# Optimization experiments

Measured on AMD Instinct MI355X. Metric: run time of the kernel, lower is better.

The kernel has to match this reference:

```python
import jax, jax.numpy as jnp
import numpy as np


def setup_inputs() -> dict:
    key = jax.random.key(0)
    k1, k2 = jax.random.split(key)
    B, S, D, E = 4, 8192, 1024, 64
    x = jax.random.normal(k1, (B, S, D), dtype=jnp.float32)
    W = jax.random.normal(k2, (E, D), dtype=jnp.float32) * (1.0 / np.sqrt(D))
    return {"x": x, "W": W, "top_k": 1}


EXPERT_CAPACITY = 640


def reference(x, W, top_k):
    # Router logits: small-dim linear (bias=False), jitter=0 so no noise.
    logits = jnp.einsum("bsd,ed->bse", x, W)              # [B,S,E]
    probs = jax.nn.softmax(logits, axis=-1)               # [B,S,E]
    num_experts = W.shape[0]
    # top-k over experts (top_k == 1 here)
    top_k_values, top_k_indices = jax.lax.top_k(probs, top_k)  # [B,S,k]
    # one-hot over experts, summed over the k slots -> [B,S,E] int mask
    expert_indices = jax.nn.one_hot(top_k_indices, num_experts, dtype=jnp.int32).sum(axis=-2)
    # token priority: running count of tokens assigned to each expert along seq
    token_priority = jnp.cumsum(expert_indices, axis=-2)  # [B,S,E]
    capacity_mask = token_priority <= EXPERT_CAPACITY
    expert_indices = expert_indices * capacity_mask.astype(jnp.int32)
    # top_k_values [B,S,1] broadcasts over E (valid only for k==1, as in torch)
    router_probs = top_k_values * expert_indices.astype(top_k_values.dtype)
    return expert_indices, router_probs, logits
```

## Files before the change

kernel.cpp:

```cpp
#include <hip/hip_runtime.h>
#include <hip/hip_bf16.h>

#define NB 4
#define NS 8192
#define ND 1024
#define NE 64
#define NM (NB * NS)
#define CAPACITY 640

#define BM 64
#define BK 64
#define NKT (ND / BK)
#define NBLK (NM / BM)
#define CPB (NS / BM)

#define OCH 64
#define NOB (NM / OCH)

typedef short short8 __attribute__((ext_vector_type(8)));
typedef float f32x4 __attribute__((ext_vector_type(4)));

#define GLOAD16(g, l)                                                          \
    __builtin_amdgcn_global_load_lds(                                          \
        (const __attribute__((address_space(1))) void*)(g),                    \
        (__attribute__((address_space(3))) void*)(l), 16, 0, 0)

__global__ __launch_bounds__(256, 2) void k1_mfma(const float* __restrict__ x,
                                                  const float* __restrict__ W,
                                                  float* __restrict__ logits,
                                                  int* __restrict__ idx_ws,
                                                  float* __restrict__ prob_ws,
                                                  int* __restrict__ hist)
{
    __shared__ char SL[65536];
    __shared__ int lh[NE];

    const int tid = threadIdx.x;
    const int lane = tid & 63;
    const int wv = tid >> 6;
    const int lr = lane & 15;
    const int kq = lane >> 4;
    const int tok0 = blockIdx.x * BM;

    if (tid < NE) lh[tid] = 0;

    f32x4 acc[4];
#pragma unroll
    for (int j = 0; j < 4; ++j) acc[j] = (f32x4){0.f, 0.f, 0.f, 0.f};

    auto stage = [&](int kt, int b) {
        const int k0 = kt * BK;
        const int half = wv & 1;
        const int r0 = half * 32 + (lane >> 4);
        const int uslot = lane & 15;
        const float* src;
        char* dst;
        if (wv < 2) {
            src = x + (size_t)(tok0)*ND;
            dst = SL + b * 16384 + half * 8192;
        } else {
            src = W;
            dst = SL + 32768 + b * 16384 + half * 8192;
        }
#pragma unroll
        for (int i = 0; i < 8; ++i) {
            const int r = r0 + i * 4;
            const int su = uslot ^ (r & 15);
            const float* g = src + (size_t)r * ND + k0 + su * 4;
            GLOAD16(g, dst + i * 1024);
        }
    };

    auto compute = [&](int b) {
        const float* xsb = (const float*)(SL + b * 16384);
        const float* wsb = (const float*)(SL + 32768 + b * 16384);
        const int arow = wv * 16 + lr;
#pragma unroll
        for (int kk = 0; kk < 2; ++kk) {
            const int su = kk * 8 + kq * 2;
            f32x4 a0 = *(const f32x4*)&xsb[arow * 64 + ((su)     ^ lr) * 4];
            f32x4 a1 = *(const f32x4*)&xsb[arow * 64 + ((su + 1) ^ lr) * 4];
            float f[8] = {a0[0], a0[1], a0[2], a0[3], a1[0], a1[1], a1[2], a1[3]};
            short8 ah, al;
#pragma unroll
            for (int c = 0; c < 8; ++c) {
                unsigned int u = __builtin_bit_cast(unsigned int, f[c]);
                ah[c] = (short)(u >> 16);
                float fhi = __builtin_bit_cast(float, u & 0xFFFF0000u);
                __hip_bfloat16 lb = __float2bfloat16(f[c] - fhi);
                al[c] = __builtin_bit_cast(short, lb);
            }
#pragma unroll
            for (int j = 0; j < 4; ++j) {
                const int erow = j * 16 + lr;
                f32x4 w0 = *(const f32x4*)&wsb[erow * 64 + ((su)     ^ lr) * 4];
                f32x4 w1 = *(const f32x4*)&wsb[erow * 64 + ((su + 1) ^ lr) * 4];
                float g[8] = {w0[0], w0[1], w0[2], w0[3], w1[0], w1[1], w1[2], w1[3]};
                short8 bh, bl;
#pragma unroll
                for (int c = 0; c < 8; ++c) {
                    __hip_bfloat16 hb = __float2bfloat16(g[c]);
                    float r = g[c] - __bfloat162float(hb);
                    __hip_bfloat16 lb = __float2bfloat16(r);
                    bh[c] = __builtin_bit_cast(short, hb);
                    bl[c] = __builtin_bit_cast(short, lb);
                }
                acc[j] = __builtin_amdgcn_mfma_f32_16x16x32_bf16(ah, bh, acc[j], 0, 0, 0);
                acc[j] = __builtin_amdgcn_mfma_f32_16x16x32_bf16(ah, bl, acc[j], 0, 0, 0);
                acc[j] = __builtin_amdgcn_mfma_f32_16x16x32_bf16(al, bh, acc[j], 0, 0, 0);
            }
        }
    };

    stage(0, 0);
#pragma unroll
    for (int kt = 0; kt < NKT; ++kt) {
        const int b = kt & 1;
        if (kt + 1 < NKT) {
            stage(kt + 1, b ^ 1);
            asm volatile("s_waitcnt vmcnt(8)" ::: "memory");
        } else {
            asm volatile("s_waitcnt vmcnt(0)" ::: "memory");
        }
        __builtin_amdgcn_s_barrier();
        __builtin_amdgcn_sched_barrier(0);
        compute(b);
        __builtin_amdgcn_sched_barrier(0);
        __builtin_amdgcn_s_barrier();
    }

    __syncthreads();

    float* sLog = (float*)SL;

#pragma unroll
    for (int r = 0; r < 4; ++r) {
        const int tl = wv * 16 + kq * 4 + r;
        float val[4];
#pragma unroll
        for (int j = 0; j < 4; ++j) val[j] = acc[j][r];

        float m = val[0];
        int mi = lr;
#pragma unroll
        for (int j = 1; j < 4; ++j) {
            if (val[j] > m) { m = val[j]; mi = j * 16 + lr; }
        }
#pragma unroll
        for (int off = 1; off < 16; off <<= 1) {
            float m2 = __shfl_xor(m, off);
            int mi2 = __shfl_xor(mi, off);
            if (m2 > m || (m2 == m && mi2 < mi)) { m = m2; mi = mi2; }
        }
        float s = 0.0f;
#pragma unroll
        for (int j = 0; j < 4; ++j) s += __expf(val[j] - m);
#pragma unroll
        for (int off = 1; off < 16; off <<= 1) s += __shfl_xor(s, off);

#pragma unroll
        for (int j = 0; j < 4; ++j) sLog[tl * NE + j * 16 + lr] = val[j];
        if (lr == 0) {
            idx_ws[tok0 + tl] = mi;
            prob_ws[tok0 + tl] = 1.0f / s;
            atomicAdd(&lh[mi], 1);
        }
    }
    __syncthreads();

    const size_t g0 = (size_t)tok0 * NE;
#pragma unroll
    for (int i = 0; i < 4; ++i) {
        const int fl = i * 1024 + tid * 4;
        *(float4*)&logits[g0 + fl] = *(const float4*)&sLog[fl];
    }
    if (tid < NE) hist[blockIdx.x * NE + tid] = lh[tid];
}

__global__ __launch_bounds__(256) void k_out(const int* __restrict__ idx_ws,
                                             const float* __restrict__ prob_ws,
                                             const int* __restrict__ hist,
                                             float* __restrict__ e_out,
                                             float* __restrict__ p_out)
{
    __shared__ int sMi[OCH];
    __shared__ float sPr[OCH];
    __shared__ int sAd[OCH];
    __shared__ int pp[4][NE];

    const int c = blockIdx.x;
    const int b = c >> 7;
    const int s = c & 127;
    const int t0 = c * OCH;
    const int tid = threadIdx.x;
    const int lane = tid & 63;
    const int wv = tid >> 6;

    if (tid < OCH) {
        sMi[tid] = idx_ws[t0 + tid];
        sPr[tid] = prob_ws[t0 + tid];
    }

    {
        int run = 0;
        const int* hrow = hist + (size_t)(b * CPB) * NE + lane;
        for (int i = wv; i < s; i += 4) run += hrow[i * NE];
        pp[wv][lane] = run;
    }
    __syncthreads();

    if (wv == 0) {
        int run = pp[0][lane] + pp[1][lane] + pp[2][lane] + pp[3][lane];
        for (int j = 0; j < OCH; ++j) {
            if (sMi[j] == lane) { ++run; sAd[j] = (run <= CAPACITY) ? 1 : 0; }
        }
    }
    __syncthreads();

    const size_t g0 = (size_t)t0 * NE;
#pragma unroll
    for (int i = 0; i < 4; ++i) {
        const int fl = i * 1024 + tid * 4;
        const int t = fl >> 6;
        const int e0 = fl & 63;
        const int mi = sMi[t];
        const float pr = sPr[t];
        const int ad = sAd[t];
        float4 ev, pv;
        float* evp = &ev.x;
        float* pvp = &pv.x;
#pragma unroll
        for (int cc = 0; cc < 4; ++cc) {
            const bool hit = (mi == e0 + cc) && ad;
            evp[cc] = hit ? 1.0f : 0.0f;
            pvp[cc] = hit ? pr : 0.0f;
        }
        *(float4*)&e_out[g0 + fl] = ev;
        *(float4*)&p_out[g0 + fl] = pv;
    }
}

extern "C" void kernel_launch(void* const* d_in, const int* in_sizes, int n_in,
                              void* d_out, int out_size, void* d_ws, size_t ws_size,
                              hipStream_t stream)
{
    const float* x = (const float*)d_in[0];
    const float* W = (const float*)d_in[1];

    float* out = (float*)d_out;
    float* e_out = out;
    float* p_out = out + (size_t)NM * NE;
    float* logits = out + 2 * (size_t)NM * NE;

    char* ws = (char*)d_ws;
    int* idx_ws    = (int*)ws;
    float* prob_ws = (float*)(ws + (size_t)NM * 4);
    int* hist      = (int*)(ws + (size_t)NM * 8);

    k1_mfma<<<NBLK, 256, 0, stream>>>(x, W, logits, idx_ws, prob_ws, hist);
    k_out<<<NOB, 256, 0, stream>>>(idx_ws, prob_ws, hist, e_out, p_out);
}
```

Measured before the change: 47.01 us.

## Shrink GEMM tile to 32 tokens with 32-wide K and two-wave blocks

Reduces the router GEMM block from 64 tokens with four waves to 32 tokens with two waves and a 32-wide K step. The staging map, LDS swizzle and logits write-out are reworked to match, and the histogram prefix in the output kernel now sums twice as many per-block entries. The aim is more blocks and higher occupancy with less LDS per block. In exchange W is re-read from global/L2 twice as often per token, and there are twice as many K iterations with barriers.

```diff
diff --git a/kernel.cpp b/kernel.cpp
--- a/kernel.cpp
+++ b/kernel.cpp
@@ -8,11 +8,11 @@
 #define NM (NB * NS)
 #define CAPACITY 640
 
-#define BM 64
-#define BK 64
+#define BM 32
+#define BK 32
 #define NKT (ND / BK)
 #define NBLK (NM / BM)
-#define CPB (NS / BM)
+#define C32PB (NS / BM)
 
 #define OCH 64
 #define NOB (NM / OCH)
@@ -25,14 +25,14 @@
         (const __attribute__((address_space(1))) void*)(g),                    \
         (__attribute__((address_space(3))) void*)(l), 16, 0, 0)
 
-__global__ __launch_bounds__(256, 2) void k1_mfma(const float* __restrict__ x,
+__global__ __launch_bounds__(128, 4) void k1_mfma(const float* __restrict__ x,
                                                   const float* __restrict__ W,
                                                   float* __restrict__ logits,
                                                   int* __restrict__ idx_ws,
                                                   float* __restrict__ prob_ws,
                                                   int* __restrict__ hist)
 {
-    __shared__ char SL[65536];
+    __shared__ char SL[24576];
     __shared__ int lh[NE];
 
     const int tid = threadIdx.x;
@@ -50,65 +50,62 @@
 
     auto stage = [&](int kt, int b) {
         const int k0 = kt * BK;
-        const int half = wv & 1;
-        const int r0 = half * 32 + (lane >> 4);
-        const int uslot = lane & 15;
-        const float* src;
-        char* dst;
-        if (wv < 2) {
-            src = x + (size_t)(tok0)*ND;
-            dst = SL + b * 16384 + half * 8192;
-        } else {
-            src = W;
-            dst = SL + 32768 + b * 16384 + half * 8192;
-        }
-#pragma unroll
-        for (int i = 0; i < 8; ++i) {
-            const int r = r0 + i * 4;
-            const int su = uslot ^ (r & 15);
-            const float* g = src + (size_t)r * ND + k0 + su * 4;
-            GLOAD16(g, dst + i * 1024);
+        const int lrow8 = lane >> 3;
+        const int uslot = lane & 7;
+        const int u0 = wv * 6;
+#pragma unroll
+        for (int q = 0; q < 6; ++q) {
+            const int u = u0 + q;
+            if (u < 4) {
+                const int r = u * 8 + lrow8;
+                const int su = uslot ^ (r & 7);
+                const float* g = x + (size_t)(tok0 + r) * ND + k0 + su * 4;
+                GLOAD16(g, SL + b * 4096 + u * 1024);
+            } else {
+                const int r = (u - 4) * 8 + lrow8;
+                const int su = uslot ^ (r & 7);
+                const float* g = W + (size_t)r * ND + k0 + su * 4;
+                GLOAD16(g, SL + 8192 + b * 8192 + (u - 4) * 1024);
+            }
         }
     };
 
     auto compute = [&](int b) {
-        const float* xsb = (const float*)(SL + b * 16384);
-        const float* wsb = (const float*)(SL + 32768 + b * 16384);
+        const float* xsb = (const float*)(SL + b * 4096);
+        const float* wsb = (const float*)(SL + 8192 + b * 8192);
         const int arow = wv * 16 + lr;
-#pragma unroll
-        for (int kk = 0; kk < 2; ++kk) {
-            const int su = kk * 8 + kq * 2;
-            f32x4 a0 = *(const f32x4*)&xsb[arow * 64 + ((su)     ^ lr) * 4];
-            f32x4 a1 = *(const f32x4*)&xsb[arow * 64 + ((su + 1) ^ lr) * 4];
-            float f[8] = {a0[0], a0[1], a0[2], a0[3], a1[0], a1[1], a1[2], a1[3]};
-            short8 ah, al;
+        const int l7 = lr & 7;
+        const int su = kq * 2;
+        f32x4 a0 = *(const f32x4*)&xsb[arow * 32 + ((su)     ^ l7) * 4];
+        f32x4 a1 = *(const f32x4*)&xsb[arow * 32 + ((su + 1) ^ l7) * 4];
+        float f[8] = {a0[0], a0[1], a0[2], a0[3], a1[0], a1[1], a1[2], a1[3]};
+        short8 ah, al;
+#pragma unroll
+        for (int c = 0; c < 8; ++c) {
+            unsigned int u = __builtin_bit_cast(unsigned int, f[c]);
+            ah[c] = (short)(u >> 16);
+            float fhi = __builtin_bit_cast(float, u & 0xFFFF0000u);
+            __hip_bfloat16 lb = __float2bfloat16(f[c] - fhi);
+            al[c] = __builtin_bit_cast(short, lb);
+        }
+#pragma unroll
+        for (int j = 0; j < 4; ++j) {
+            const int erow = j * 16 + lr;
+            f32x4 w0 = *(const f32x4*)&wsb[erow * 32 + ((su)     ^ l7) * 4];
+            f32x4 w1 = *(const f32x4*)&wsb[erow * 32 + ((su + 1) ^ l7) * 4];
+            float g[8] = {w0[0], w0[1], w0[2], w0[3], w1[0], w1[1], w1[2], w1[3]};
+            short8 bh, bl;
 #pragma unroll
             for (int c = 0; c < 8; ++c) {
-                unsigned int u = __builtin_bit_cast(unsigned int, f[c]);
-                ah[c] = (short)(u >> 16);
-                float fhi = __builtin_bit_cast(float, u & 0xFFFF0000u);
-                __hip_bfloat16 lb = __float2bfloat16(f[c] - fhi);
-                al[c] = __builtin_bit_cast(short, lb);
+                __hip_bfloat16 hb = __float2bfloat16(g[c]);
+                float r = g[c] - __bfloat162float(hb);
+                __hip_bfloat16 lb = __float2bfloat16(r);
+                bh[c] = __builtin_bit_cast(short, hb);
+                bl[c] = __builtin_bit_cast(short, lb);
             }
-#pragma unroll
-            for (int j = 0; j < 4; ++j) {
-                const int erow = j * 16 + lr;
-                f32x4 w0 = *(const f32x4*)&wsb[erow * 64 + ((su)     ^ lr) * 4];
-                f32x4 w1 = *(const f32x4*)&wsb[erow * 64 + ((su + 1) ^ lr) * 4];
-                float g[8] = {w0[0], w0[1], w0[2], w0[3], w1[0], w1[1], w1[2], w1[3]};
-                short8 bh, bl;
-#pragma unroll
-                for (int c = 0; c < 8; ++c) {
-                    __hip_bfloat16 hb = __float2bfloat16(g[c]);
-                    float r = g[c] - __bfloat162float(hb);
-                    __hip_bfloat16 lb = __float2bfloat16(r);
-                    bh[c] = __builtin_bit_cast(short, hb);
-                    bl[c] = __builtin_bit_cast(short, lb);
-                }
-                acc[j] = __builtin_amdgcn_mfma_f32_16x16x32_bf16(ah, bh, acc[j], 0, 0, 0);
-                acc[j] = __builtin_amdgcn_mfma_f32_16x16x32_bf16(ah, bl, acc[j], 0, 0, 0);
-                acc[j] = __builtin_amdgcn_mfma_f32_16x16x32_bf16(al, bh, acc[j], 0, 0, 0);
-            }
+            acc[j] = __builtin_amdgcn_mfma_f32_16x16x32_bf16(ah, bh, acc[j], 0, 0, 0);
+            acc[j] = __builtin_amdgcn_mfma_f32_16x16x32_bf16(ah, bl, acc[j], 0, 0, 0);
+            acc[j] = __builtin_amdgcn_mfma_f32_16x16x32_bf16(al, bh, acc[j], 0, 0, 0);
         }
     };
 
@@ -118,7 +115,7 @@
         const int b = kt & 1;
         if (kt + 1 < NKT) {
             stage(kt + 1, b ^ 1);
-            asm volatile("s_waitcnt vmcnt(8)" ::: "memory");
+            asm volatile("s_waitcnt vmcnt(6)" ::: "memory");
         } else {
             asm volatile("s_waitcnt vmcnt(0)" ::: "memory");
         }
@@ -171,7 +168,7 @@
     const size_t g0 = (size_t)tok0 * NE;
 #pragma unroll
     for (int i = 0; i < 4; ++i) {
-        const int fl = i * 1024 + tid * 4;
+        const int fl = i * 512 + tid * 4;
         *(float4*)&logits[g0 + fl] = *(const float4*)&sLog[fl];
     }
     if (tid < NE) hist[blockIdx.x * NE + tid] = lh[tid];
@@ -203,8 +200,9 @@
 
     {
         int run = 0;
-        const int* hrow = hist + (size_t)(b * CPB) * NE + lane;
-        for (int i = wv; i < s; i += 4) run += hrow[i * NE];
+        const int* hrow = hist + (size_t)(b * C32PB) * NE + lane;
+        const int n = 2 * s;
+        for (int i = wv; i < n; i += 4) run += hrow[i * NE];
         pp[wv][lane] = run;
     }
     __syncthreads();
@@ -257,6 +255,6 @@
     float* prob_ws = (float*)(ws + (size_t)NM * 4);
     int* hist      = (int*)(ws + (size_t)NM * 8);
 
-    k1_mfma<<<NBLK, 256, 0, stream>>>(x, W, logits, idx_ws, prob_ws, hist);
+    k1_mfma<<<NBLK, 128, 0, stream>>>(x, W, logits, idx_ws, prob_ws, hist);
     k_out<<<NOB, 256, 0, stream>>>(idx_ws, prob_ws, hist, e_out, p_out);
 }
```

Measured after the change: 60.69 us. +29.1%, slower.

## Triple-buffer x tiles and stage W through registers in GEMM pipeline

Applied to the files above, without the earlier changes.

The x tiles now go through a three-deep LDS ring filled by direct global-to-LDS loads, so waves 0-1 keep two tiles in flight. The W tile is loaded into registers by waves 2-3 and written into a single LDS buffer after each compute step. The goal is to hide more of the x streaming latency and free LDS space for the third x buffer. The cost is extra register pressure, a serialized W write after each barrier, and a possible race where W is overwritten before all waves finish reading it.

```diff
diff --git a/kernel.cpp b/kernel.cpp
--- a/kernel.cpp
+++ b/kernel.cpp
@@ -48,32 +48,43 @@
 #pragma unroll
     for (int j = 0; j < 4; ++j) acc[j] = (f32x4){0.f, 0.f, 0.f, 0.f};
 
-    auto stage = [&](int kt, int b) {
+    const int xr0 = (wv & 1) * 32 + (lane >> 4);
+    const int xslot = lane & 15;
+    auto stage_x = [&](int kt) {
         const int k0 = kt * BK;
-        const int half = wv & 1;
-        const int r0 = half * 32 + (lane >> 4);
-        const int uslot = lane & 15;
-        const float* src;
-        char* dst;
-        if (wv < 2) {
-            src = x + (size_t)(tok0)*ND;
-            dst = SL + b * 16384 + half * 8192;
-        } else {
-            src = W;
-            dst = SL + 32768 + b * 16384 + half * 8192;
-        }
+        char* dst = SL + (kt % 3) * 16384 + (wv & 1) * 8192;
 #pragma unroll
         for (int i = 0; i < 8; ++i) {
-            const int r = r0 + i * 4;
-            const int su = uslot ^ (r & 15);
-            const float* g = src + (size_t)r * ND + k0 + su * 4;
+            const int r = xr0 + i * 4;
+            const int su = xslot ^ (r & 15);
+            const float* g = x + (size_t)(tok0 + r) * ND + k0 + su * 4;
             GLOAD16(g, dst + i * 1024);
         }
     };
 
-    auto compute = [&](int b) {
-        const float* xsb = (const float*)(SL + b * 16384);
-        const float* wsb = (const float*)(SL + 32768 + b * 16384);
+    const int wrow0 = (wv & 1) * 32 + (lane >> 4);
+    const int wunit = lane & 15;
+    float4 wreg[8];
+    auto loadW = [&](int kt) {
+        const int k0 = kt * BK;
+#pragma unroll
+        for (int i = 0; i < 8; ++i) {
+            const int r = wrow0 + i * 4;
+            wreg[i] = *(const float4*)(W + (size_t)r * ND + k0 + wunit * 4);
+        }
+    };
+    auto writeW = [&]() {
+        char* wb = SL + 49152;
+#pragma unroll
+        for (int i = 0; i < 8; ++i) {
+            const int r = wrow0 + i * 4;
+            *(float4*)(wb + r * 256 + ((wunit ^ (r & 15)) * 16)) = wreg[i];
+        }
+    };
+
+    auto compute = [&](int kt) {
+        const float* xsb = (const float*)(SL + (kt % 3) * 16384);
+        const float* wsb = (const float*)(SL + 49152);
         const int arow = wv * 16 + lr;
 #pragma unroll
         for (int kk = 0; kk < 2; ++kk) {
@@ -112,21 +123,36 @@
         }
     };
 
-    stage(0, 0);
+    if (wv < 2) {
+        stage_x(0);
+        stage_x(1);
+    } else {
+        loadW(0);
+        asm volatile("s_waitcnt vmcnt(0)" ::: "memory");
+        writeW();
+        asm volatile("s_waitcnt lgkmcnt(0)" ::: "memory");
+    }
+
 #pragma unroll
     for (int kt = 0; kt < NKT; ++kt) {
-        const int b = kt & 1;
-        if (kt + 1 < NKT) {
-            stage(kt + 1, b ^ 1);
-            asm volatile("s_waitcnt vmcnt(8)" ::: "memory");
+        if (wv < 2) {
+            if (kt + 2 < NKT) stage_x(kt + 2);
+            if (kt < NKT - 2)      asm volatile("s_waitcnt vmcnt(16)" ::: "memory");
+            else if (kt == NKT - 2) asm volatile("s_waitcnt vmcnt(8)" ::: "memory");
+            else                    asm volatile("s_waitcnt vmcnt(0)" ::: "memory");
         } else {
-            asm volatile("s_waitcnt vmcnt(0)" ::: "memory");
+            if (kt + 1 < NKT) loadW(kt + 1);
+            asm volatile("s_waitcnt lgkmcnt(0)" ::: "memory");
         }
         __builtin_amdgcn_s_barrier();
         __builtin_amdgcn_sched_barrier(0);
-        compute(b);
+        compute(kt);
         __builtin_amdgcn_sched_barrier(0);
         __builtin_amdgcn_s_barrier();
+        if (wv >= 2 && kt + 1 < NKT) {
+            asm volatile("s_waitcnt vmcnt(0)" ::: "memory");
+            writeW();
+        }
     }
 
     __syncthreads();
```

Result: slower. 69.53 us (+47.9%).
